# Optimization experiments

Measured on AMD Instinct MI355X. Metric: run time of the kernel, lower is better.

## Reference

```python
import jax, jax.numpy as jnp
import numpy as np

A4 = 0.1
EPS = 1e-8  # torch.cosine_similarity eps


def setup_inputs() -> dict:
    key = jax.random.key(0)
    ks = jax.random.split(key, 7)
    N, D, C = 200000, 256, 7
    return {
        "seq": jax.random.normal(ks[0], (N, D), jnp.float32),
        "seq1": jax.random.normal(ks[1], (N, D), jnp.float32),
        "prompt": jax.random.normal(ks[2], (3, D), jnp.float32),
        "w_np": jnp.array([[0.5, 0.4, 0.3]], jnp.float32),  # weighted_prompt init
        "w_ds": jax.random.normal(ks[4], (1, D), jnp.float32) * 0.05,  # downstreamprompt weight
        "w_df": jnp.array([[0.0, 1.0]], jnp.float32),  # weighted_feature init
        "ave": jax.random.normal(ks[6], (C, D), jnp.float32),  # class prototypes (train=0)
    }


def reference(seq, seq1, prompt, w_np, w_ds, w_df, ave):
    # weighted_prompt -> ELU -> 1 + .
    weight = 1.0 + jax.nn.elu(w_np @ prompt)          # [1, D]
    rawret1 = weight * seq                             # [N, D]
    rawret2 = w_ds * seq                               # downstreamprompt
    rawret3 = jax.nn.elu(w_df[0, 0] * rawret1 + w_df[0, 1] * rawret2)
    rawret = rawret3 + A4 * seq1                       # [N, D]
    # per-row cosine similarity vs each class prototype, then softmax
    dots = rawret @ ave.T                              # [N, C]
    nr = jnp.linalg.norm(rawret, axis=1, keepdims=True)   # [N, 1]
    na = jnp.linalg.norm(ave, axis=1)                     # [C]
    sims = dots / jnp.maximum(nr * na[None, :], EPS)
    return jax.nn.softmax(sims, axis=1)
```

## Files before the change

kernel.cpp:

```cpp
#include <hip/hip_runtime.h>
#include <math.h>


__device__ __forceinline__ float elu1(float x) {
    return x > 0.0f ? x : __expf(x) - 1.0f;
}

__device__ __forceinline__ float wave_sum(float v) {
#pragma unroll
    for (int off = 32; off > 0; off >>= 1)
        v += __shfl_xor(v, off, 64);
    return v;
}

__global__ __launch_bounds__(256) void downprompt_kernel(
    const float* __restrict__ seq,
    const float* __restrict__ seq1,
    const float* __restrict__ prompt,
    const float* __restrict__ w_np,
    const float* __restrict__ w_ds,
    const float* __restrict__ w_df,
    const float* __restrict__ ave,
    float* __restrict__ out,
    int N)
{
    __shared__ float s_coef[256];
    __shared__ float s_ave[7][256];

    const int tid  = threadIdx.x;
    const int lane = tid & 63;

    {
        const float a  = w_df[0];
        const float b  = w_df[1];
        const float w0 = w_np[0], w1 = w_np[1], w2 = w_np[2];
        const float pr = w0 * prompt[tid] + w1 * prompt[256 + tid]
                       + w2 * prompt[512 + tid];
        s_coef[tid] = a * (1.0f + elu1(pr)) + b * w_ds[tid];
#pragma unroll
        for (int c = 0; c < 7; ++c)
            s_ave[c][tid] = ave[c * 256 + tid];
    }
    __syncthreads();

    float na[7];
#pragma unroll
    for (int c = 0; c < 7; ++c) {
        const float4 v = *(const float4*)&s_ave[c][lane << 2];
        na[c] = sqrtf(wave_sum(v.x * v.x + v.y * v.y + v.z * v.z + v.w * v.w));
    }

    const int q   = lane & 3;
    const int sub = lane >> 2;
    const int wavesPerBlock = blockDim.x >> 6;
    const int gwave = blockIdx.x * wavesPerBlock + (tid >> 6);
    const int nwave = gridDim.x * wavesPerBlock;
    const int ngroups = (N + 15) >> 4;

    for (int g = gwave; g < ngroups; g += nwave) {
        const int row = (g << 4) + sub;
        if (row >= N) continue;

        const float* ps = seq  + (size_t)row * 256;
        const float* pt = seq1 + (size_t)row * 256;

        float acc[8];
#pragma unroll
        for (int k = 0; k < 8; ++k) acc[k] = 0.0f;

#pragma unroll 4
        for (int i = 0; i < 16; ++i) {
            const int col = (i << 4) + (q << 2);
            const float4 s  = *(const float4*)(ps + col);
            const float4 t  = *(const float4*)(pt + col);
            const float4 cf = *(const float4*)&s_coef[col];

            const float r0 = elu1(cf.x * s.x) + 0.1f * t.x;
            const float r1 = elu1(cf.y * s.y) + 0.1f * t.y;
            const float r2 = elu1(cf.z * s.z) + 0.1f * t.z;
            const float r3 = elu1(cf.w * s.w) + 0.1f * t.w;

            acc[7] += r0 * r0 + r1 * r1 + r2 * r2 + r3 * r3;
#pragma unroll
            for (int c = 0; c < 7; ++c) {
                const float4 av = *(const float4*)&s_ave[c][col];
                acc[c] += r0 * av.x + r1 * av.y + r2 * av.z + r3 * av.w;
            }
        }

#pragma unroll
        for (int off = 1; off <= 2; off <<= 1) {
#pragma unroll
            for (int k = 0; k < 8; ++k)
                acc[k] += __shfl_xor(acc[k], off, 64);
        }

        const float nr = sqrtf(acc[7]);
        float sims[7];
        float m = -INFINITY;
#pragma unroll
        for (int c = 0; c < 7; ++c) {
            const float den = fmaxf(nr * na[c], 1e-8f);
            sims[c] = acc[c] * __builtin_amdgcn_rcpf(den);
            m = fmaxf(m, sims[c]);
        }
        float e[7], sum = 0.0f;
#pragma unroll
        for (int c = 0; c < 7; ++c) {
            e[c] = __expf(sims[c] - m);
            sum += e[c];
        }
        const float inv = __builtin_amdgcn_rcpf(sum);

        const float eq  = (q == 0) ? e[0] : (q == 1) ? e[1]
                        : (q == 2) ? e[2] : e[3];
        const float eq4 = (q == 0) ? e[4] : (q == 1) ? e[5] : e[6];

        float* po = out + (size_t)row * 7;
        po[q] = eq * inv;
        if (q < 3) po[q + 4] = eq4 * inv;
    }
}

extern "C" void kernel_launch(void* const* d_in, const int* in_sizes, int n_in,
                              void* d_out, int out_size, void* d_ws, size_t ws_size,
                              hipStream_t stream) {
    const float* seq    = (const float*)d_in[0];
    const float* seq1   = (const float*)d_in[1];
    const float* prompt = (const float*)d_in[2];
    const float* w_np   = (const float*)d_in[3];
    const float* w_ds   = (const float*)d_in[4];
    const float* w_df   = (const float*)d_in[5];
    const float* ave    = (const float*)d_in[6];
    float* out = (float*)d_out;

    const int N = in_sizes[0] / 256;
    const int ngroups = (N + 15) / 16;
    const int wavesPerBlock = 4;
    int blocks = (ngroups + wavesPerBlock * 2 - 1) / (wavesPerBlock * 2);
    if (blocks < 1) blocks = 1;

    downprompt_kernel<<<blocks, 256, 0, stream>>>(seq, seq1, prompt, w_np, w_ds,
                                                  w_df, ave, out, N);
}
```

Measured before the change: 431.7 us.

## Stream row chunks through per-wave LDS ring with async global-to-LDS loads

Replaces direct global float4 loads of seq and seq1 with global_load_lds async copies into a three-slot per-wave LDS ring. Loads are issued three chunks ahead and gated by explicit vmcnt waits, so memory latency overlaps compute. The grid is doubled so each wave handles about one group instead of two. This raises LDS use to about 24KB per block and adds waits, which may reduce occupancy, and correctness depends on how async LDS writes map lanes to addresses.

```diff
diff --git a/kernel.cpp b/kernel.cpp
--- a/kernel.cpp
+++ b/kernel.cpp
@@ -1,6 +1,15 @@
 #include <hip/hip_runtime.h>
 #include <math.h>
 
+
+typedef __attribute__((address_space(1))) const float gbl_float;
+typedef __attribute__((address_space(3))) float lds_float;
+
+#define ASYNC16(gp, lp) \
+    __builtin_amdgcn_global_load_lds((gbl_float*)(gp), (lds_float*)(lp), 16, 0, 0)
+
+#define VMW(N) asm volatile("s_waitcnt vmcnt(" #N ")" ::: "memory")
+#define LGKW   asm volatile("s_waitcnt lgkmcnt(0)" ::: "memory")
 
 __device__ __forceinline__ float elu1(float x) {
     return x > 0.0f ? x : __expf(x) - 1.0f;
@@ -26,9 +35,11 @@
 {
     __shared__ float s_coef[256];
     __shared__ float s_ave[7][256];
+    __shared__ float s_ring[4][1536];
 
     const int tid  = threadIdx.x;
     const int lane = tid & 63;
+    const int w    = tid >> 6;
 
     {
         const float a  = w_df[0];
@@ -51,42 +62,62 @@
     }
 
     const int q   = lane & 3;
+    const int q4  = q << 2;
+    const int l4  = lane << 2;
     const int sub = lane >> 2;
     const int wavesPerBlock = blockDim.x >> 6;
     const int gwave = blockIdx.x * wavesPerBlock + (tid >> 6);
     const int nwave = gridDim.x * wavesPerBlock;
     const int ngroups = (N + 15) >> 4;
 
+    float* const ring = &s_ring[w][0];
+
     for (int g = gwave; g < ngroups; g += nwave) {
         const int row = (g << 4) + sub;
         if (row >= N) continue;
 
-        const float* ps = seq  + (size_t)row * 256;
-        const float* pt = seq1 + (size_t)row * 256;
+        const float* ps = seq  + (size_t)row * 256 + q4;
+        const float* pt = seq1 + (size_t)row * 256 + q4;
+
+        ASYNC16(ps +  0, ring +    0);
+        ASYNC16(pt +  0, ring +  256);
+        ASYNC16(ps + 16, ring +  512);
+        ASYNC16(pt + 16, ring +  768);
+        ASYNC16(ps + 32, ring + 1024);
+        ASYNC16(pt + 32, ring + 1280);
 
         float acc[8];
 #pragma unroll
         for (int k = 0; k < 8; ++k) acc[k] = 0.0f;
 
-#pragma unroll 4
-        for (int i = 0; i < 16; ++i) {
-            const int col = (i << 4) + (q << 2);
-            const float4 s  = *(const float4*)(ps + col);
-            const float4 t  = *(const float4*)(pt + col);
-            const float4 cf = *(const float4*)&s_coef[col];
+#define ITER(J, WN) do {                                                  \
+        VMW(WN);                                                          \
+        const float4 s = *(const float4*)(ring + ((J) % 3) * 512 + l4);   \
+        const float4 t = *(const float4*)(ring + ((J) % 3) * 512 + 256 + l4); \
+        LGKW;         \
+        if ((J) <= 12) {                                                  \
+            ASYNC16(ps + ((J) + 3) * 16, ring + ((J) % 3) * 512);         \
+            ASYNC16(pt + ((J) + 3) * 16, ring + ((J) % 3) * 512 + 256);   \
+        }                                                                 \
+        const int col = ((J) << 4) + q4;                                  \
+        const float4 cf = *(const float4*)&s_coef[col];                   \
+        const float r0 = elu1(cf.x * s.x) + 0.1f * t.x;                   \
+        const float r1 = elu1(cf.y * s.y) + 0.1f * t.y;                   \
+        const float r2 = elu1(cf.z * s.z) + 0.1f * t.z;                   \
+        const float r3 = elu1(cf.w * s.w) + 0.1f * t.w;                   \
+        acc[7] += r0 * r0 + r1 * r1 + r2 * r2 + r3 * r3;                  \
+        _Pragma("unroll")                                                 \
+        for (int c = 0; c < 7; ++c) {                                     \
+            const float4 av = *(const float4*)&s_ave[c][col];             \
+            acc[c] += r0 * av.x + r1 * av.y + r2 * av.z + r3 * av.w;      \
+        }                                                                 \
+    } while (0)
 
-            const float r0 = elu1(cf.x * s.x) + 0.1f * t.x;
-            const float r1 = elu1(cf.y * s.y) + 0.1f * t.y;
-            const float r2 = elu1(cf.z * s.z) + 0.1f * t.z;
-            const float r3 = elu1(cf.w * s.w) + 0.1f * t.w;
-
-            acc[7] += r0 * r0 + r1 * r1 + r2 * r2 + r3 * r3;
-#pragma unroll
-            for (int c = 0; c < 7; ++c) {
-                const float4 av = *(const float4*)&s_ave[c][col];
-                acc[c] += r0 * av.x + r1 * av.y + r2 * av.z + r3 * av.w;
-            }
-        }
+        ITER( 0, 4); ITER( 1, 4); ITER( 2, 4); ITER( 3, 4);
+        ITER( 4, 4); ITER( 5, 4); ITER( 6, 4); ITER( 7, 4);
+        ITER( 8, 4); ITER( 9, 4); ITER(10, 4); ITER(11, 4);
+        ITER(12, 4); ITER(13, 4); ITER(14, 2); ITER(15, 0);
+#undef ITER
 
 #pragma unroll
         for (int off = 1; off <= 2; off <<= 1) {
@@ -137,7 +168,7 @@
     const int N = in_sizes[0] / 256;
     const int ngroups = (N + 15) / 16;
     const int wavesPerBlock = 4;
-    int blocks = (ngroups + wavesPerBlock * 2 - 1) / (wavesPerBlock * 2);
+    int blocks = (ngroups + wavesPerBlock - 1) / wavesPerBlock;
     if (blocks < 1) blocks = 1;
 
     downprompt_kernel<<<blocks, 256, 0, stream>>>(seq, seq1, prompt, w_np, w_ds,
```

After: 415.2 us. -3.8%, faster.
